# Kernel optimization log

Hardware: AMD Instinct MI355X
Metric: run time of the kernel (lower is better)

Reference implementation:

```python
import jax, jax.numpy as jnp
import numpy as np

TAU = 0.07
MARGIN = 0.2
NUM_SPECIES = 64  # matches fill_max of species_ids


def _l2norm(x):
    return x / jnp.linalg.norm(x, axis=-1, keepdims=True)


def setup_inputs() -> dict:
    key = jax.random.key(0)
    k1, k2, k3 = jax.random.split(key, 3)
    B, D = 8192, 256
    species_embed = _l2norm(jax.random.normal(k1, (B, D), dtype=jnp.float32))
    text_embed = _l2norm(jax.random.normal(k2, (B, D), dtype=jnp.float32))
    species_ids = jax.random.randint(k3, (B,), 0, NUM_SPECIES, dtype=jnp.int32)
    return {"species_embed": species_embed, "text_embed": text_embed,
            "species_ids": species_ids}


def reference(species_embed, text_embed, species_ids):
    B = species_embed.shape[0]
    dtype = species_embed.dtype

    sim = species_embed @ text_embed.T                      # (B, B)
    same = species_ids[:, None] == species_ids[None, :]     # (B, B) bool, symmetric
    diag_sim = jnp.diagonal(sim)                            # (B,)

    # ---- intra-species symmetric InfoNCE (per-species CE, averaged over species)
    logits = sim / TAU
    neg_inf = jnp.finfo(dtype).min
    masked = jnp.where(same, logits, neg_inf)               # restrict to same-species cols
    diag_logit = diag_sim / TAU
    ce_v2t = jax.scipy.special.logsumexp(masked, axis=1) - diag_logit   # per-row CE
    ce_t2v = jax.scipy.special.logsumexp(masked.T, axis=1) - diag_logit # transpose: same mask is symmetric

    ones = jnp.ones((B,), dtype=dtype)
    counts = jax.ops.segment_sum(ones, species_ids, num_segments=NUM_SPECIES)          # group sizes
    seg_v2t = jax.ops.segment_sum(ce_v2t, species_ids, num_segments=NUM_SPECIES)
    seg_t2v = jax.ops.segment_sum(ce_t2v, species_ids, num_segments=NUM_SPECIES)
    valid_s = counts >= 2                                   # groups with <2 members skipped
    per_species = (seg_v2t + seg_t2v) / (2.0 * jnp.maximum(counts, 1.0))
    n_valid = jnp.maximum(jnp.sum(valid_s.astype(dtype)), 1.0)
    loss_infonce = jnp.sum(jnp.where(valid_s, per_species, 0.0)) / n_valid

    # ---- cross-species triplet (pos = mean same-species sim excl. self, neg = mean diff-species sim)
    same_f = same.astype(dtype)
    row_same_sum = jnp.sum(sim * same_f, axis=1)            # includes diagonal
    row_sum = jnp.sum(sim, axis=1)
    pos_cnt = jnp.sum(same_f, axis=1) - 1.0
    neg_cnt = B - jnp.sum(same_f, axis=1)
    pos_mean = (row_same_sum - diag_sim) / jnp.maximum(pos_cnt, 1.0)
    neg_mean = (row_sum - row_same_sum) / jnp.maximum(neg_cnt, 1.0)
    tri = jax.nn.relu(neg_mean - pos_mean + MARGIN)
    valid_i = (pos_cnt > 0) & (neg_cnt > 0)
    n_valid_i = jnp.maximum(jnp.sum(valid_i.astype(dtype)), 1.0)
    loss_triplet = jnp.sum(jnp.where(valid_i, tri, 0.0)) / n_valid_i

    return loss_infonce + loss_triplet
```

## Files before the change

kernel.cpp:

```cpp
#include <hip/hip_runtime.h>
#include <hip/hip_fp16.h>

#define TAU 0.07f
#define MARGIN 0.2f
#define NSPEC 64
#define BB 8192
#define DD 256

#define WS_SCALARS   0
#define WS_COUNTS    64
#define WS_OFFSETS   320
#define WS_LSEROW    1024
#define WS_LSECOL    33792
#define WS_TS        66560
#define WS_T         132096
#define WS_MEMBER    133120
#define ZERO_F4      8256

typedef _Float16 half8 __attribute__((ext_vector_type(8)));
typedef float float4v __attribute__((ext_vector_type(4)));
typedef unsigned int uint4v __attribute__((ext_vector_type(4)));

__device__ __forceinline__ uint4v pack8(float4 a, float4 b) {
  half8 h;
  h[0] = (_Float16)a.x; h[1] = (_Float16)a.y; h[2] = (_Float16)a.z; h[3] = (_Float16)a.w;
  h[4] = (_Float16)b.x; h[5] = (_Float16)b.y; h[6] = (_Float16)b.z; h[7] = (_Float16)b.w;
  return __builtin_bit_cast(uint4v, h);
}

__device__ __forceinline__ float dot4(float4 a, float4 b) {
  return a.x * b.x + a.y * b.y + a.z * b.z + a.w * b.w;
}

__global__ void k1_all(const int* __restrict__ ids, int* counts_g, int* offsets_g,
                       int* memberList, float* scalars, char* ws) {
  __shared__ int cnt[NSPEC];
  __shared__ int off[NSPEC];
  int tid = threadIdx.x;
  float4v z4 = {0.f, 0.f, 0.f, 0.f};
  float4v* zb = (float4v*)(ws + WS_LSEROW);
  for (int u = tid; u < ZERO_F4; u += 1024) zb[u] = z4;
  if (tid < 16) ((unsigned*)ws)[tid] = 0u;
  if (tid < NSPEC) cnt[tid] = 0;
  __syncthreads();
  int myS[8], myP[8];
  #pragma unroll
  for (int r = 0; r < 8; ++r) {
    int i = r * 1024 + tid;
    int s = ids[i];
    myS[r] = s;
    myP[r] = atomicAdd(&cnt[s], 1);
  }
  __syncthreads();
  if (tid < NSPEC) {
    int o = 0;
    for (int t = 0; t < NSPEC; ++t) o += (t < tid) ? cnt[t] : 0;
    off[tid] = o;
    offsets_g[tid] = o;
    int c = cnt[tid];
    counts_g[tid] = c;
    unsigned long long bv = __ballot(c >= 2);
    float nvi = (c >= 2 && c <= BB - 1) ? (float)c : 0.f;
    for (int o2 = 1; o2 < 64; o2 <<= 1) nvi += __shfl_xor(nvi, o2);
    if (tid == 0) {
      scalars[2] = (float)__popcll(bv);
      scalars[3] = nvi;
    }
  }
  __syncthreads();
  #pragma unroll
  for (int r = 0; r < 8; ++r) {
    int i = r * 1024 + tid;
    memberList[off[myS[r]] + myP[r]] = i;
  }
}

__global__ void kmid(const float* __restrict__ sp, const float* __restrict__ tx,
                     const int* __restrict__ counts, const int* __restrict__ offsets,
                     const int* __restrict__ memberList,
                     float* Ts, float* T, float* lseRow, float* lseCol) {
  __shared__ uint4v lds5[1536];
  int bid = blockIdx.x;
  int tid = threadIdx.x;

  if (bid >= 512) {
    int v = bid - 512;
    int s = v & 63, r = v >> 6;
    int m = counts[s], g0 = offsets[s];
    int k0 = (m * r) >> 3, k1e = (m * (r + 1)) >> 3;
    if (k0 >= k1e) return;
    int d = tid;
    float acc = 0.f;
    for (int k = k0; k < k1e; ++k) acc += tx[memberList[g0 + k] * DD + d];
    atomicAdd(&Ts[s * DD + d], acc);
    atomicAdd(&T[d], acc);
    return;
  }

  int s = bid & 63;
  int m = counts[s];
  int g0 = offsets[s];
  int lane = tid & 63, wv = tid >> 6;
  int quad = lane >> 4, cl = lane & 15;
  int rt0 = (bid >> 6) & 3, ct0 = (bid >> 8) & 1;

  for (int rt = rt0; rt * 64 < m; rt += 4) {
    for (int ct = ct0; ct * 128 < m; ct += 2) {
      float4v acc[8];
      #pragma unroll
      for (int cf = 0; cf < 8; ++cf) acc[cf] = (float4v){0.f, 0.f, 0.f, 0.f};

      for (int kc = 0; kc < 4; ++kc) {
        __syncthreads();
        #pragma unroll
        for (int p = 0; p < 6; ++p) {
          int u = p * 256 + tid;
          int isB = u >= 512;
          int v = isB ? (u - 512) : u;
          int row = v >> 3;
          int sub = v & 7;
          int ksl = sub >> 2, q = sub & 3;
          int d0 = kc * 64 + ksl * 32 + q * 8;
          int idx = isB ? (ct * 128 + row) : (rt * 64 + row);
          uint4v val = (uint4v){0u, 0u, 0u, 0u};
          if (idx < m) {
            const float* src = (isB ? tx : sp) + memberList[g0 + idx] * DD + d0;
            float4 f0 = *reinterpret_cast<const float4*>(src);
            float4 f1 = *reinterpret_cast<const float4*>(src + 4);
            val = pack8(f0, f1);
          }
          int dst = isB ? (512 + (ksl * 128 + row) * 4 + q)
                        : ((ksl * 64 + row) * 4 + q);
          lds5[dst] = val;
        }
        __syncthreads();
        #pragma unroll
        for (int ksl = 0; ksl < 2; ++ksl) {
          half8 a = __builtin_bit_cast(half8, lds5[(ksl * 64 + wv * 16 + cl) * 4 + quad]);
          #pragma unroll
          for (int cf = 0; cf < 8; ++cf) {
            half8 b = __builtin_bit_cast(half8, lds5[512 + (ksl * 128 + cf * 16 + cl) * 4 + quad]);
            acc[cf] = __builtin_amdgcn_mfma_f32_16x16x32_f16(a, b, acc[cf], 0, 0, 0);
          }
        }
      }

      int riBase = rt * 64 + wv * 16 + quad * 4;
      float rowAcc[4] = {0.f, 0.f, 0.f, 0.f};
      #pragma unroll
      for (int cf = 0; cf < 8; ++cf) {
        int ci = ct * 128 + cf * 16 + cl;
        bool cv = ci < m;
        float colAcc = 0.f;
        #pragma unroll
        for (int reg = 0; reg < 4; ++reg) {
          bool rv = (riBase + reg) < m;
          float e = (rv && cv) ? __expf(acc[cf][reg] * (1.f / TAU)) : 0.f;
          rowAcc[reg] += e;
          colAcc += e;
        }
        colAcc += __shfl_xor(colAcc, 16);
        colAcc += __shfl_xor(colAcc, 32);
        if (quad == 0 && cv) atomicAdd(&lseCol[g0 + ci], colAcc);
      }
      #pragma unroll
      for (int reg = 0; reg < 4; ++reg) {
        float v = rowAcc[reg];
        v += __shfl_xor(v, 1);
        v += __shfl_xor(v, 2);
        v += __shfl_xor(v, 4);
        v += __shfl_xor(v, 8);
        if (cl == 0 && (riBase + reg) < m) atomicAdd(&lseRow[g0 + riBase + reg], v);
      }
    }
  }
}

__global__ void kend(const float* __restrict__ sp, const float* __restrict__ tx,
                     const int* __restrict__ ids, const int* __restrict__ counts,
                     const int* __restrict__ memberList,
                     const float* __restrict__ Ts, const float* __restrict__ T,
                     const float* __restrict__ lseRow, const float* __restrict__ lseCol,
                     float* scalars, float* out) {
  __shared__ float red[32];
  int tid = threadIdx.x;
  int gt = blockIdx.x * 1024 + tid;
  int g = gt >> 6, lane = gt & 63;
  int i = memberList[g];
  int s = ids[i];
  int m = counts[s];
  float4 a = *reinterpret_cast<const float4*>(sp + i * DD + lane * 4);
  float4 b = *reinterpret_cast<const float4*>(tx + i * DD + lane * 4);
  float4 c = *reinterpret_cast<const float4*>(Ts + s * DD + lane * 4);
  float4 tv = *reinterpret_cast<const float4*>(T + lane * 4);
  float dDiag = dot4(a, b);
  float dTs   = dot4(a, c);
  float dT    = dot4(a, tv);
  #pragma unroll
  for (int o = 1; o < 64; o <<= 1) {
    dDiag += __shfl_xor(dDiag, o);
    dTs   += __shfl_xor(dTs, o);
    dT    += __shfl_xor(dT, o);
  }
  if (lane == 0) {
    float term = 0.f, tri = 0.f;
    if (m >= 2) {
      term = (__logf(lseRow[g]) + __logf(lseCol[g]) - 2.f * dDiag * (1.f / TAU)) /
             (2.f * (float)m);
      float posMean = (dTs - dDiag) / fmaxf((float)(m - 1), 1.f);
      float negMean = (dT - dTs) / fmaxf((float)(BB - m), 1.f);
      if (m <= BB - 1) tri = fmaxf(negMean - posMean + MARGIN, 0.f);
    }
    int wv = tid >> 6;
    red[wv] = term;
    red[16 + wv] = tri;
  }
  __syncthreads();
  if (tid == 0) {
    float infoS = 0.f, triS = 0.f;
    #pragma unroll
    for (int w = 0; w < 16; ++w) { infoS += red[w]; triS += red[16 + w]; }
    atomicAdd(&scalars[1], infoS);
    atomicAdd(&scalars[0], triS);
    __threadfence();
    unsigned prev = atomicAdd((unsigned*)&scalars[4], 1u);
    if (prev == (unsigned)(gridDim.x - 1)) {
      float fi = atomicAdd(&scalars[1], 0.f);
      float ft = atomicAdd(&scalars[0], 0.f);
      float nv = scalars[2];
      float nvi = scalars[3];
      out[0] = fi / fmaxf(nv, 1.f) + ft / fmaxf(nvi, 1.f);
    }
  }
}

extern "C" void kernel_launch(void* const* d_in, const int* in_sizes, int n_in,
                              void* d_out, int out_size, void* d_ws, size_t ws_size,
                              hipStream_t stream) {
  const float* sp = (const float*)d_in[0];
  const float* tx = (const float*)d_in[1];
  const int* ids = (const int*)d_in[2];
  float* out = (float*)d_out;

  char* ws = (char*)d_ws;
  float* scalars = (float*)(ws + WS_SCALARS);
  int* counts = (int*)(ws + WS_COUNTS);
  int* offsets = (int*)(ws + WS_OFFSETS);
  float* lseRow = (float*)(ws + WS_LSEROW);
  float* lseCol = (float*)(ws + WS_LSECOL);
  float* Ts = (float*)(ws + WS_TS);
  float* T = (float*)(ws + WS_T);
  int* memberList = (int*)(ws + WS_MEMBER);

  k1_all<<<1, 1024, 0, stream>>>(ids, counts, offsets, memberList, scalars, ws);
  kmid<<<1024, 256, 0, stream>>>(sp, tx, counts, offsets, memberList, Ts, T,
                                 lseRow, lseCol);
  kend<<<512, 1024, 0, stream>>>(sp, tx, ids, counts, memberList, Ts, T,
                                 lseRow, lseCol, scalars, out);
}
```

Baseline: 122.0 us.

## Prefetch member rows into registers, move zeroing to memset, split total-sum blocks

Gathered row indices for a tile are now cached once in shared memory. The global loads for the next k-chunk are issued into registers before the MFMA work on the current chunk, so load latency overlaps compute. Workspace zeroing moves from the single-block k1_all kernel to hipMemsetAsync, and the counts and offsets arrays are relocated outside the zeroed range. The global column sum T is now computed by 32 extra contiguous-read blocks instead of atomics from every per-species block, and the per-species gather loop is unrolled by four. The register prefetch raises register pressure, and the memset adds one more operation on the stream.

```diff
diff --git a/kernel.cpp b/kernel.cpp
--- a/kernel.cpp
+++ b/kernel.cpp
@@ -8,14 +8,14 @@
 #define DD 256
 
 #define WS_SCALARS   0
-#define WS_COUNTS    64
-#define WS_OFFSETS   320
 #define WS_LSEROW    1024
 #define WS_LSECOL    33792
 #define WS_TS        66560
 #define WS_T         132096
+#define WS_ZERO_BYTES 133120
 #define WS_MEMBER    133120
-#define ZERO_F4      8256
+#define WS_COUNTS    165888
+#define WS_OFFSETS   166144
 
 typedef _Float16 half8 __attribute__((ext_vector_type(8)));
 typedef float float4v __attribute__((ext_vector_type(4)));
@@ -33,14 +33,10 @@
 }
 
 __global__ void k1_all(const int* __restrict__ ids, int* counts_g, int* offsets_g,
-                       int* memberList, float* scalars, char* ws) {
+                       int* memberList, float* scalars) {
   __shared__ int cnt[NSPEC];
   __shared__ int off[NSPEC];
   int tid = threadIdx.x;
-  float4v z4 = {0.f, 0.f, 0.f, 0.f};
-  float4v* zb = (float4v*)(ws + WS_LSEROW);
-  for (int u = tid; u < ZERO_F4; u += 1024) zb[u] = z4;
-  if (tid < 16) ((unsigned*)ws)[tid] = 0u;
   if (tid < NSPEC) cnt[tid] = 0;
   __syncthreads();
   int myS[8], myP[8];
@@ -79,21 +75,42 @@
                      const int* __restrict__ counts, const int* __restrict__ offsets,
                      const int* __restrict__ memberList,
                      float* Ts, float* T, float* lseRow, float* lseCol) {
-  __shared__ uint4v lds5[1536];
+  __shared__ uint4v frag[1536];
+  __shared__ int idx[192];
   int bid = blockIdx.x;
   int tid = threadIdx.x;
 
+  if (bid >= 1024) {
+    int r0 = (bid - 1024) * 256;
+    int d = tid;
+    float acc = 0.f;
+    #pragma unroll 8
+    for (int rr = 0; rr < 256; ++rr) acc += tx[(r0 + rr) * DD + d];
+    atomicAdd(&T[d], acc);
+    return;
+  }
   if (bid >= 512) {
-    int v = bid - 512;
-    int s = v & 63, r = v >> 6;
+    int v2 = bid - 512;
+    int s = v2 & 63, r = v2 >> 6;
     int m = counts[s], g0 = offsets[s];
     int k0 = (m * r) >> 3, k1e = (m * (r + 1)) >> 3;
     if (k0 >= k1e) return;
     int d = tid;
     float acc = 0.f;
-    for (int k = k0; k < k1e; ++k) acc += tx[memberList[g0 + k] * DD + d];
+    int k = k0;
+    for (; k + 4 <= k1e; k += 4) {
+      int i0 = memberList[g0 + k];
+      int i1 = memberList[g0 + k + 1];
+      int i2 = memberList[g0 + k + 2];
+      int i3 = memberList[g0 + k + 3];
+      float a0 = tx[i0 * DD + d];
+      float a1 = tx[i1 * DD + d];
+      float a2 = tx[i2 * DD + d];
+      float a3 = tx[i3 * DD + d];
+      acc += a0 + a1 + a2 + a3;
+    }
+    for (; k < k1e; ++k) acc += tx[memberList[g0 + k] * DD + d];
     atomicAdd(&Ts[s * DD + d], acc);
-    atomicAdd(&T[d], acc);
     return;
   }
 
@@ -106,40 +123,60 @@
 
   for (int rt = rt0; rt * 64 < m; rt += 4) {
     for (int ct = ct0; ct * 128 < m; ct += 2) {
+      __syncthreads();
+      if (tid < 192) {
+        int base = (tid < 64) ? (rt * 64 + tid) : (ct * 128 + (tid - 64));
+        idx[tid] = (base < m) ? memberList[g0 + base] : -1;
+      }
+      __syncthreads();
+
+      const float* srcB[6];
+      bool val[6];
+      int dst[6];
+      float4 r0[6], r1[6];
+      #pragma unroll
+      for (int p = 0; p < 6; ++p) {
+        int u = p * 256 + tid;
+        int isB = u >= 512;
+        int v = isB ? (u - 512) : u;
+        int row = v >> 3, sub = v & 7;
+        int ksl = sub >> 2, q = sub & 3;
+        int ridx = idx[isB ? (64 + row) : row];
+        val[p] = ridx >= 0;
+        srcB[p] = (isB ? tx : sp) + (val[p] ? ridx : 0) * DD + ksl * 32 + q * 8;
+        dst[p] = isB ? (512 + (ksl * 128 + row) * 4 + q)
+                     : ((ksl * 64 + row) * 4 + q);
+      }
+      #pragma unroll
+      for (int p = 0; p < 6; ++p) {
+        r0[p] = *reinterpret_cast<const float4*>(srcB[p]);
+        r1[p] = *reinterpret_cast<const float4*>(srcB[p] + 4);
+      }
+
       float4v acc[8];
       #pragma unroll
       for (int cf = 0; cf < 8; ++cf) acc[cf] = (float4v){0.f, 0.f, 0.f, 0.f};
 
       for (int kc = 0; kc < 4; ++kc) {
         __syncthreads();
+        uint4v z4 = (uint4v){0u, 0u, 0u, 0u};
         #pragma unroll
-        for (int p = 0; p < 6; ++p) {
-          int u = p * 256 + tid;
-          int isB = u >= 512;
-          int v = isB ? (u - 512) : u;
-          int row = v >> 3;
-          int sub = v & 7;
-          int ksl = sub >> 2, q = sub & 3;
-          int d0 = kc * 64 + ksl * 32 + q * 8;
-          int idx = isB ? (ct * 128 + row) : (rt * 64 + row);
-          uint4v val = (uint4v){0u, 0u, 0u, 0u};
-          if (idx < m) {
-            const float* src = (isB ? tx : sp) + memberList[g0 + idx] * DD + d0;
-            float4 f0 = *reinterpret_cast<const float4*>(src);
-            float4 f1 = *reinterpret_cast<const float4*>(src + 4);
-            val = pack8(f0, f1);
+        for (int p = 0; p < 6; ++p)
+          frag[dst[p]] = val[p] ? pack8(r0[p], r1[p]) : z4;
+        __syncthreads();
+        if (kc < 3) {
+          #pragma unroll
+          for (int p = 0; p < 6; ++p) {
+            r0[p] = *reinterpret_cast<const float4*>(srcB[p] + (kc + 1) * 64);
+            r1[p] = *reinterpret_cast<const float4*>(srcB[p] + (kc + 1) * 64 + 4);
           }
-          int dst = isB ? (512 + (ksl * 128 + row) * 4 + q)
-                        : ((ksl * 64 + row) * 4 + q);
-          lds5[dst] = val;
         }
-        __syncthreads();
         #pragma unroll
         for (int ksl = 0; ksl < 2; ++ksl) {
-          half8 a = __builtin_bit_cast(half8, lds5[(ksl * 64 + wv * 16 + cl) * 4 + quad]);
+          half8 a = __builtin_bit_cast(half8, frag[(ksl * 64 + wv * 16 + cl) * 4 + quad]);
           #pragma unroll
           for (int cf = 0; cf < 8; ++cf) {
-            half8 b = __builtin_bit_cast(half8, lds5[512 + (ksl * 128 + cf * 16 + cl) * 4 + quad]);
+            half8 b = __builtin_bit_cast(half8, frag[512 + (ksl * 128 + cf * 16 + cl) * 4 + quad]);
             acc[cf] = __builtin_amdgcn_mfma_f32_16x16x32_f16(a, b, acc[cf], 0, 0, 0);
           }
         }
@@ -244,16 +281,17 @@
 
   char* ws = (char*)d_ws;
   float* scalars = (float*)(ws + WS_SCALARS);
-  int* counts = (int*)(ws + WS_COUNTS);
-  int* offsets = (int*)(ws + WS_OFFSETS);
   float* lseRow = (float*)(ws + WS_LSEROW);
   float* lseCol = (float*)(ws + WS_LSECOL);
   float* Ts = (float*)(ws + WS_TS);
   float* T = (float*)(ws + WS_T);
   int* memberList = (int*)(ws + WS_MEMBER);
-
-  k1_all<<<1, 1024, 0, stream>>>(ids, counts, offsets, memberList, scalars, ws);
-  kmid<<<1024, 256, 0, stream>>>(sp, tx, counts, offsets, memberList, Ts, T,
+  int* counts = (int*)(ws + WS_COUNTS);
+  int* offsets = (int*)(ws + WS_OFFSETS);
+
+  hipMemsetAsync(d_ws, 0, WS_ZERO_BYTES, stream);
+  k1_all<<<1, 1024, 0, stream>>>(ids, counts, offsets, memberList, scalars);
+  kmid<<<1056, 256, 0, stream>>>(sp, tx, counts, offsets, memberList, Ts, T,
                                  lseRow, lseCol);
   kend<<<512, 1024, 0, stream>>>(sp, tx, ids, counts, memberList, Ts, T,
                                  lseRow, lseCol, scalars, out);
```

After: 112.0 us. -8.2%, faster.
